# Kernel tuning notes

Measured on AMD Instinct MI355X. Metric: run time of the kernel, lower is better.

## Reference

```python
import jax, jax.numpy as jnp
import numpy as np

N = 3000          # num_nodes
B = 1             # batch
T_IN = 12
T_OUT = 12
F_IN = 2
F_OUT = 2
HEADS = 8
HID = 32          # hidden_dim (GAT out channels, LSTM hidden)
E = 32000         # directed edges (before self-loops)
NEG_SLOPE = 0.2   # PyG GATConv leaky_relu slope


def setup_inputs() -> dict:
    key = jax.random.key(0)
    ks = jax.random.split(key, 20)
    s = 0.1
    inp = {
        "X": jax.random.normal(ks[0], (B, N, T_IN, F_IN), jnp.float32),
        "edge_index": jax.random.randint(ks[1], (2, E), 0, N, dtype=jnp.int64),
        # GATConv params (shared lin for src/dst, concat=False -> bias of size HID)
        "gat_w": jax.random.normal(ks[2], (HEADS * HID, F_IN), jnp.float32) * s,
        "att_src": jax.random.normal(ks[3], (HEADS, HID), jnp.float32) * s,
        "att_dst": jax.random.normal(ks[4], (HEADS, HID), jnp.float32) * s,
        "gat_b": jax.random.normal(ks[5], (HID,), jnp.float32) * s,
        # 2-layer LSTM, PyTorch gate order (i, f, g, o)
        "w_ih0": jax.random.normal(ks[6], (4 * HID, HID), jnp.float32) * s,
        "w_hh0": jax.random.normal(ks[7], (4 * HID, HID), jnp.float32) * s,
        "b_ih0": jax.random.normal(ks[8], (4 * HID,), jnp.float32) * s,
        "b_hh0": jax.random.normal(ks[9], (4 * HID,), jnp.float32) * s,
        "w_ih1": jax.random.normal(ks[10], (4 * HID, HID), jnp.float32) * s,
        "w_hh1": jax.random.normal(ks[11], (4 * HID, HID), jnp.float32) * s,
        "b_ih1": jax.random.normal(ks[12], (4 * HID,), jnp.float32) * s,
        "b_hh1": jax.random.normal(ks[13], (4 * HID,), jnp.float32) * s,
        # final head: HID -> F_OUT * T_OUT
        "fc_w": jax.random.normal(ks[14], (F_OUT * T_OUT, HID), jnp.float32) * s,
        "fc_b": jax.random.normal(ks[15], (F_OUT * T_OUT,), jnp.float32) * s,
    }
    return inp


def _lstm_layer(xs, w_ih, w_hh, b_ih, b_hh):
    # xs: (T, BN, D) -> hidden states (T, BN, H)
    Hd = w_hh.shape[1]
    def step(carry, x):
        h, c = carry
        g = x @ w_ih.T + h @ w_hh.T + b_ih + b_hh
        i, f, gg, o = jnp.split(g, 4, axis=-1)
        c = jax.nn.sigmoid(f) * c + jax.nn.sigmoid(i) * jnp.tanh(gg)
        h = jax.nn.sigmoid(o) * jnp.tanh(c)
        return (h, c), h
    z = jnp.zeros((xs.shape[1], Hd), xs.dtype)
    _, hs = jax.lax.scan(step, (z, z), xs)
    return hs


def reference(X, edge_index, gat_w, att_src, att_dst, gat_b,
              w_ih0, w_hh0, b_ih0, b_hh0, w_ih1, w_hh1, b_ih1, b_hh1,
              fc_w, fc_b):
    Bb, Nn, T, F = X.shape
    BN = Bb * Nn
    H, C = att_src.shape

    # (T, BN, F), all timesteps processed at once (GAT params shared across t)
    Xr = X.transpose(2, 0, 1, 3).reshape(T, BN, F)
    h = (Xr @ gat_w.T).reshape(T, BN, H, C)          # shared lin for src/dst
    a_s = (h * att_src).sum(-1)                      # (T, BN, H)
    a_d = (h * att_dst).sum(-1)

    # add self-loops (PyG GATConv default) over all BN nodes
    loops = jnp.arange(BN, dtype=edge_index.dtype)
    src = jnp.concatenate([edge_index[0], loops])
    dst = jnp.concatenate([edge_index[1], loops])

    # edge attention logits, edge axis leading for segment ops: (Etot, T, H)
    e = jax.nn.leaky_relu(a_s[:, src] + a_d[:, dst], NEG_SLOPE)
    e = jnp.moveaxis(e, 1, 0)

    # segment softmax over incoming edges per destination node
    m = jax.ops.segment_max(e, dst, num_segments=BN)
    ex = jnp.exp(e - m[dst])
    den = jax.ops.segment_sum(ex, dst, num_segments=BN)
    alpha = ex / den[dst]                            # (Etot, T, H)

    h_node = jnp.moveaxis(h, 0, 1)                   # (BN, T, H, C)
    msg = alpha[..., None] * h_node[src]             # (Etot, T, H, C)
    agg = jax.ops.segment_sum(msg, dst, num_segments=BN)  # (BN, T, H, C)
    gat_out = agg.mean(2) + gat_b                    # concat=False -> head mean; (BN, T, C)

    # 2-layer LSTM over time
    xs = gat_out.transpose(1, 0, 2)                  # (T, BN, C)
    hs = _lstm_layer(xs, w_ih0, w_hh0, b_ih0, b_hh0)
    hs = _lstm_layer(hs, w_ih1, w_hh1, b_ih1, b_hh1)
    h_last = hs[-1]                                  # (BN, HID)

    out = h_last @ fc_w.T + fc_b                     # (BN, F_OUT*T_OUT)
    return out.reshape(Bb, Nn, T_OUT, F)
```

## Files before the change

### kernel.cpp

```cpp
#include <hip/hip_runtime.h>
#include <math.h>

#define N_NODES 3000
#define T_STEPS 12
#define F_INP 2
#define HEADS 8
#define HID 32
#define E_EDGES 32000
#define E_TOT (E_EDGES + N_NODES)
#define NEG_SLOPE 0.2f
#define OUT_F 24
#define CHUNKS 8
#define NT (N_NODES * T_STEPS)
#define WROW 33

__device__ __forceinline__ float sigm(float x) {
    return 1.0f / (1.0f + __expf(-x));
}
__device__ __forceinline__ float tanh_f(float x) {
    return 1.0f - 2.0f / (__expf(2.0f * x) + 1.0f);
}
__device__ __forceinline__ float rdlane(float v, int l) {
    return __int_as_float(__builtin_amdgcn_readlane(__float_as_int(v), l));
}

__global__ void k_init(int* __restrict__ deg,
                       const float* __restrict__ gat_w,
                       const float* __restrict__ att_src,
                       const float* __restrict__ att_dst,
                       float* __restrict__ proj,
                       const float* __restrict__ X,
                       float2* __restrict__ Xt) {
    int b = blockIdx.x;
    if (b < 12) {
        int i = b * 256 + threadIdx.x;
        if (i < N_NODES) deg[i] = 0;
    } else if (b == 12) {
        int tid = threadIdx.x;
        if (tid < 32) {
            int h = tid & 7, w = tid >> 3;
            const float* att = (w < 2) ? att_src : att_dst;
            int f = w & 1;
            float s = 0.0f;
            for (int c = 0; c < 32; c++)
                s += gat_w[((h * 32 + c) * 2) + f] * att[h * 32 + c];
            proj[w * 8 + h] = s;
        }
    } else {
        int i = (b - 13) * 256 + threadIdx.x;
        if (i < NT) {
            int n = i / T_STEPS, t = i - n * T_STEPS;
            float2 v = *(const float2*)&X[(size_t)i * 2];
            Xt[(size_t)t * N_NODES + n] = v;
        }
    }
}

__global__ void k_deg(const int* __restrict__ ei, int* __restrict__ deg) {
    int i = blockIdx.x * blockDim.x + threadIdx.x;
    if (i >= E_TOT) return;
    int d = (i < E_EDGES) ? ei[E_EDGES + i] : (i - E_EDGES);
    atomicAdd(&deg[d], 1);
}

__global__ __launch_bounds__(256) void k_scan(const int* __restrict__ deg,
                                              int* __restrict__ row_start,
                                              int* __restrict__ cursor) {
    __shared__ int part[256];
    int tid = threadIdx.x;
    const int CH = (N_NODES + 255) / 256;
    int base = tid * CH;
    int s = 0;
    for (int i = 0; i < CH; i++) {
        int idx = base + i;
        if (idx < N_NODES) s += deg[idx];
    }
    part[tid] = s;
    __syncthreads();
    if (tid == 0) {
        int run = 0;
        for (int i = 0; i < 256; i++) { int tmp = part[i]; part[i] = run; run += tmp; }
        row_start[N_NODES] = run;
    }
    __syncthreads();
    int off = part[tid];
    for (int i = 0; i < CH; i++) {
        int idx = base + i;
        if (idx < N_NODES) {
            row_start[idx] = off;
            cursor[idx] = off;
            off += deg[idx];
        }
    }
}

__global__ void k_scatter(const int* __restrict__ ei, int* __restrict__ cursor,
                          int* __restrict__ csr_src) {
    int i = blockIdx.x * blockDim.x + threadIdx.x;
    if (i >= E_TOT) return;
    int s, d;
    if (i < E_EDGES) { s = ei[i]; d = ei[E_EDGES + i]; }
    else             { s = i - E_EDGES; d = s; }
    int pos = atomicAdd(&cursor[d], 1);
    csr_src[pos] = s;
}

__global__ __launch_bounds__(256) void k_gat(const float2* __restrict__ Xt,
                                             const int* __restrict__ row_start,
                                             const int* __restrict__ csr_src,
                                             const float* __restrict__ proj,
                                             const float* __restrict__ gat_w,
                                             const float* __restrict__ gat_b,
                                             float* __restrict__ gat_out) {
    int pair = blockIdx.x * 4 + (threadIdx.x >> 6);
    int t = pair / N_NODES, n = pair - t * N_NODES;
    int lane = threadIdx.x & 63;
    int h = lane >> 3, slot = lane & 7;
    int rs = row_start[n];
    int deg = row_start[n + 1] - rs;
    const float2* Xp = Xt + (size_t)t * N_NODES;
    float ps0 = proj[h], ps1 = proj[8 + h];
    float pd0 = proj[16 + h], pd1 = proj[24 + h];
    float2 xd = Xp[n];
    float ad = fmaf(xd.x, pd0, xd.y * pd1);

    float x0c[CHUNKS], x1c[CHUNKS], sc[CHUNKS];
    float m = -1e30f;
    #pragma unroll
    for (int c = 0; c < CHUNKS; c++) {
        if (8 * c < deg) {
            int e = slot + 8 * c;
            int idx = rs + (e < deg ? e : deg - 1);
            int src = csr_src[idx];
            float2 xv = Xp[src];
            x0c[c] = xv.x; x1c[c] = xv.y;
            float s = fmaf(xv.x, ps0, fmaf(xv.y, ps1, ad));
            s = (s > 0.0f) ? s : NEG_SLOPE * s;
            sc[c] = (e < deg) ? s : -1e30f;
            m = fmaxf(m, sc[c]);
        } else { x0c[c] = 0.0f; x1c[c] = 0.0f; sc[c] = -1e30f; }
    }
    for (int e = 64 + slot; e < deg; e += 8) {
        float2 xv = Xp[csr_src[rs + e]];
        float s = fmaf(xv.x, ps0, fmaf(xv.y, ps1, ad));
        s = (s > 0.0f) ? s : NEG_SLOPE * s;
        m = fmaxf(m, s);
    }
    m = fmaxf(m, __shfl_xor(m, 1, 64));
    m = fmaxf(m, __shfl_xor(m, 2, 64));
    m = fmaxf(m, __shfl_xor(m, 4, 64));

    float den = 0.0f, S0 = 0.0f, S1 = 0.0f;
    #pragma unroll
    for (int c = 0; c < CHUNKS; c++) {
        if (8 * c < deg) {
            float a = __expf(sc[c] - m);
            den += a;
            S0 = fmaf(a, x0c[c], S0);
            S1 = fmaf(a, x1c[c], S1);
        }
    }
    for (int e = 64 + slot; e < deg; e += 8) {
        float2 xv = Xp[csr_src[rs + e]];
        float s = fmaf(xv.x, ps0, fmaf(xv.y, ps1, ad));
        s = (s > 0.0f) ? s : NEG_SLOPE * s;
        float a = __expf(s - m);
        den += a; S0 = fmaf(a, xv.x, S0); S1 = fmaf(a, xv.y, S1);
    }
    #pragma unroll
    for (int mm = 1; mm <= 4; mm <<= 1) {
        den += __shfl_xor(den, mm, 64);
        S0  += __shfl_xor(S0,  mm, 64);
        S1  += __shfl_xor(S1,  mm, 64);
    }
    float inv = 0.125f / den;
    float v0 = S0 * inv, v1 = S1 * inv;

    float a0[HEADS], a1[HEADS];
    #pragma unroll
    for (int hh = 0; hh < HEADS; hh++) {
        a0[hh] = rdlane(v0, hh * 8);
        a1[hh] = rdlane(v1, hh * 8);
    }

    int cc = lane & 31;
    float acc = gat_b[cc];
    #pragma unroll
    for (int hh = 0; hh < HEADS; hh++) {
        float2 g = *(const float2*)&gat_w[(hh * 32 + cc) * 2];
        acc = fmaf(a0[hh], g.x, fmaf(a1[hh], g.y, acc));
    }
    if (lane < 32)
        gat_out[((size_t)n * T_STEPS + t) * HID + cc] = acc;
}

__global__ __launch_bounds__(256, 3)
void k_lstm(const float* __restrict__ gat_out,
            const float* __restrict__ w_ih0,
            const float* __restrict__ w_hh0,
            const float* __restrict__ b_ih0,
            const float* __restrict__ b_hh0,
            const float* __restrict__ w_ih1,
            const float* __restrict__ w_hh1,
            const float* __restrict__ b_ih1,
            const float* __restrict__ b_hh1,
            const float* __restrict__ fc_w,
            const float* __restrict__ fc_b,
            float* __restrict__ out) {
    __shared__ float wl[128 * WROW];
    int tid = threadIdx.x;
    int lane = tid & 63;
    int n = blockIdx.x * 4 + (tid >> 6);
    int j = lane & 31, half = lane >> 5;
    int rowA = half * 64 + j;
    int rowB = rowA + 32;

    auto stage = [&](const float* __restrict__ src, int nfloats) {
        for (int base = tid * 4; base < nfloats; base += 1024) {
            float4 v = *(const float4*)&src[base];
            float* d = &wl[(base >> 5) * WROW + (base & 31)];
            d[0] = v.x; d[1] = v.y; d[2] = v.z; d[3] = v.w;
        }
    };
    auto loadrows = [&](float* wA, float* wB) {
        #pragma unroll
        for (int k = 0; k < 32; k++) wA[k] = wl[rowA * WROW + k];
        #pragma unroll
        for (int k = 0; k < 32; k++) wB[k] = wl[rowB * WROW + k];
    };

    float wA[32], wB[32];

    stage(w_ih0, 4096);
    __syncthreads();
    loadrows(wA, wB);
    float bA = b_ih0[rowA] + b_hh0[rowA];
    float bB = b_ih0[rowB] + b_hh0[rowB];
    float xrow[T_STEPS];
    #pragma unroll
    for (int t = 0; t < T_STEPS; t++)
        xrow[t] = gat_out[((size_t)n * T_STEPS + t) * HID + j];
    float gxa[T_STEPS], gxb[T_STEPS];
    #pragma unroll
    for (int t = 0; t < T_STEPS; t++) {
        float a = bA, b = bB;
        #pragma unroll
        for (int k = 0; k < 32; k++) {
            float xk = rdlane(xrow[t], k);
            a = fmaf(xk, wA[k], a);
            b = fmaf(xk, wB[k], b);
        }
        gxa[t] = a; gxb[t] = b;
    }
    __syncthreads();

    stage(w_hh0, 4096);
    __syncthreads();
    loadrows(wA, wB);
    float h = 0.0f, c = 0.0f;
    float h0s[T_STEPS];
    #pragma unroll
    for (int t = 0; t < T_STEPS; t++) {
        float gA0 = gxa[t], gB0 = gxb[t], gA1 = 0.0f, gB1 = 0.0f;
        #pragma unroll
        for (int k = 0; k < 16; k++) {
            float h0 = rdlane(h, k), h1 = rdlane(h, k + 16);
            gA0 = fmaf(h0, wA[k], gA0);      gA1 = fmaf(h1, wA[k + 16], gA1);
            gB0 = fmaf(h0, wB[k], gB0);      gB1 = fmaf(h1, wB[k + 16], gB1);
        }
        float gA = gA0 + gA1, gB = gB0 + gB1;
        float oA = __shfl_xor(gA, 32, 64);
        float oB = __shfl_xor(gB, 32, 64);
        float gi = half ? oA : gA;
        float gf = half ? oB : gB;
        float gg = half ? gA : oA;
        float go = half ? gB : oB;
        c = sigm(gf) * c + sigm(gi) * tanh_f(gg);
        h = sigm(go) * tanh_f(c);
        h0s[t] = h;
    }
    __syncthreads();

    stage(w_ih1, 4096);
    __syncthreads();
    loadrows(wA, wB);
    float bA1 = b_ih1[rowA] + b_hh1[rowA];
    float bB1 = b_ih1[rowB] + b_hh1[rowB];
    #pragma unroll
    for (int t = 0; t < T_STEPS; t++) {
        float a = bA1, b = bB1;
        #pragma unroll
        for (int k = 0; k < 32; k++) {
            float xk = rdlane(h0s[t], k);
            a = fmaf(xk, wA[k], a);
            b = fmaf(xk, wB[k], b);
        }
        gxa[t] = a; gxb[t] = b;
    }
    __syncthreads();

    stage(w_hh1, 4096);
    __syncthreads();
    loadrows(wA, wB);
    h = 0.0f; c = 0.0f;
    #pragma unroll
    for (int t = 0; t < T_STEPS; t++) {
        float gA0 = gxa[t], gB0 = gxb[t], gA1 = 0.0f, gB1 = 0.0f;
        #pragma unroll
        for (int k = 0; k < 16; k++) {
            float h0 = rdlane(h, k), h1 = rdlane(h, k + 16);
            gA0 = fmaf(h0, wA[k], gA0);      gA1 = fmaf(h1, wA[k + 16], gA1);
            gB0 = fmaf(h0, wB[k], gB0);      gB1 = fmaf(h1, wB[k + 16], gB1);
        }
        float gA = gA0 + gA1, gB = gB0 + gB1;
        float oA = __shfl_xor(gA, 32, 64);
        float oB = __shfl_xor(gB, 32, 64);
        float gi = half ? oA : gA;
        float gf = half ? oB : gB;
        float gg = half ? gA : oA;
        float go = half ? gB : oB;
        c = sigm(gf) * c + sigm(gi) * tanh_f(gg);
        h = sigm(go) * tanh_f(c);
    }
    __syncthreads();

    stage(fc_w, OUT_F * HID);
    __syncthreads();
    int o = (lane < OUT_F) ? lane : (OUT_F - 1);
    float acc = fc_b[o];
    #pragma unroll
    for (int k = 0; k < 32; k++) {
        float hk = rdlane(h, k);
        acc = fmaf(hk, wl[o * WROW + k], acc);
    }
    if (lane < OUT_F) out[(size_t)n * OUT_F + lane] = acc;
}

extern "C" void kernel_launch(void* const* d_in, const int* in_sizes, int n_in,
                              void* d_out, int out_size, void* d_ws, size_t ws_size,
                              hipStream_t stream) {
    (void)in_sizes; (void)n_in; (void)out_size; (void)ws_size;
    const float* X       = (const float*)d_in[0];
    const int*   ei      = (const int*)d_in[1];
    const float* gat_w   = (const float*)d_in[2];
    const float* att_src = (const float*)d_in[3];
    const float* att_dst = (const float*)d_in[4];
    const float* gat_b   = (const float*)d_in[5];
    const float* w_ih0   = (const float*)d_in[6];
    const float* w_hh0   = (const float*)d_in[7];
    const float* b_ih0   = (const float*)d_in[8];
    const float* b_hh0   = (const float*)d_in[9];
    const float* w_ih1   = (const float*)d_in[10];
    const float* w_hh1   = (const float*)d_in[11];
    const float* b_ih1   = (const float*)d_in[12];
    const float* b_hh1   = (const float*)d_in[13];
    const float* fc_w    = (const float*)d_in[14];
    const float* fc_b    = (const float*)d_in[15];
    float* out = (float*)d_out;

    char* ws = (char*)d_ws;
    size_t off = 0;
    auto alloc_f = [&](size_t n) { float* p = (float*)(ws + off); off += n * sizeof(float); return p; };
    auto alloc_i = [&](size_t n) { int* p = (int*)(ws + off); off += n * sizeof(int); return p; };

    float*  gat_out = alloc_f((size_t)NT * HID);
    float2* Xt      = (float2*)alloc_f((size_t)NT * 2);
    float*  proj    = alloc_f(32);
    int* deg       = alloc_i(N_NODES);
    int* row_start = alloc_i(N_NODES + 1);
    int* cursor    = alloc_i(N_NODES);
    int* csr_src   = alloc_i(E_TOT);

    k_init<<<13 + (NT + 255) / 256, 256, 0, stream>>>(deg, gat_w, att_src, att_dst,
                                                      proj, X, Xt);
    k_deg<<<(E_TOT + 255) / 256, 256, 0, stream>>>(ei, deg);
    k_scan<<<1, 256, 0, stream>>>(deg, row_start, cursor);
    k_scatter<<<(E_TOT + 255) / 256, 256, 0, stream>>>(ei, cursor, csr_src);
    k_gat<<<NT / 4, 256, 0, stream>>>(Xt, row_start, csr_src, proj,
                                      gat_w, gat_b, gat_out);
    k_lstm<<<N_NODES / 4, 256, 0, stream>>>(gat_out, w_ih0, w_hh0, b_ih0, b_hh0,
                                            w_ih1, w_hh1, b_ih1, b_hh1,
                                            fc_w, fc_b, out);
}
```

Measured before the change: 165.5 us.

## Fuse CSR build into single-block shared-memory kernel alongside transpose and projection

```diff
diff --git a/kernel.cpp b/kernel.cpp
--- a/kernel.cpp
+++ b/kernel.cpp
@@ -24,19 +24,67 @@
     return __int_as_float(__builtin_amdgcn_readlane(__float_as_int(v), l));
 }
 
-__global__ void k_init(int* __restrict__ deg,
-                       const float* __restrict__ gat_w,
-                       const float* __restrict__ att_src,
-                       const float* __restrict__ att_dst,
-                       float* __restrict__ proj,
-                       const float* __restrict__ X,
-                       float2* __restrict__ Xt) {
-    int b = blockIdx.x;
-    if (b < 12) {
-        int i = b * 256 + threadIdx.x;
-        if (i < N_NODES) deg[i] = 0;
-    } else if (b == 12) {
-        int tid = threadIdx.x;
+__global__ __launch_bounds__(1024) void k_graph(const int* __restrict__ ei,
+                                                const float* __restrict__ X,
+                                                const float* __restrict__ gat_w,
+                                                const float* __restrict__ att_src,
+                                                const float* __restrict__ att_dst,
+                                                float2* __restrict__ Xt,
+                                                float* __restrict__ proj,
+                                                int* __restrict__ row_start,
+                                                int* __restrict__ csr_src) {
+    int tid = threadIdx.x, b = blockIdx.x;
+    if (b == 0) {
+        __shared__ int sdeg[N_NODES];
+        __shared__ int wsum[17];
+        for (int i = tid; i < N_NODES; i += 1024) sdeg[i] = 0;
+        __syncthreads();
+        for (int i = tid; i < E_TOT; i += 1024) {
+            int d = (i < E_EDGES) ? ei[E_EDGES + i] : (i - E_EDGES);
+            atomicAdd(&sdeg[d], 1);
+        }
+        __syncthreads();
+        int base = tid * 3;
+        int d0 = (base     < N_NODES) ? sdeg[base]     : 0;
+        int d1 = (base + 1 < N_NODES) ? sdeg[base + 1] : 0;
+        int d2 = (base + 2 < N_NODES) ? sdeg[base + 2] : 0;
+        int s = d0 + d1 + d2;
+        int incl = s;
+        #pragma unroll
+        for (int dlt = 1; dlt < 64; dlt <<= 1) {
+            int v = __shfl_up(incl, dlt, 64);
+            if ((tid & 63) >= dlt) incl += v;
+        }
+        int wid = tid >> 6;
+        if ((tid & 63) == 63) wsum[wid] = incl;
+        __syncthreads();
+        if (tid == 0) {
+            int run = 0;
+            #pragma unroll
+            for (int w = 0; w < 16; w++) { int t2 = wsum[w]; wsum[w] = run; run += t2; }
+        }
+        __syncthreads();
+        int off = wsum[wid] + (incl - s);
+        if (base     < N_NODES) { row_start[base]     = off;           sdeg[base]     = off; }
+        if (base + 1 < N_NODES) { row_start[base + 1] = off + d0;      sdeg[base + 1] = off + d0; }
+        if (base + 2 < N_NODES) { row_start[base + 2] = off + d0 + d1; sdeg[base + 2] = off + d0 + d1; }
+        if (tid == 0) row_start[N_NODES] = E_TOT;
+        __syncthreads();
+        for (int i = tid; i < E_TOT; i += 1024) {
+            int s2, d;
+            if (i < E_EDGES) { s2 = ei[i]; d = ei[E_EDGES + i]; }
+            else             { s2 = i - E_EDGES; d = s2; }
+            int pos = atomicAdd(&sdeg[d], 1);
+            csr_src[pos] = s2;
+        }
+    } else if (b <= 36) {
+        int i = (b - 1) * 1024 + tid;
+        if (i < NT) {
+            int n = i / T_STEPS, t = i - n * T_STEPS;
+            float2 v = *(const float2*)&X[(size_t)i * 2];
+            Xt[(size_t)t * N_NODES + n] = v;
+        }
+    } else {
         if (tid < 32) {
             int h = tid & 7, w = tid >> 3;
             const float* att = (w < 2) ? att_src : att_dst;
@@ -46,63 +94,7 @@
                 s += gat_w[((h * 32 + c) * 2) + f] * att[h * 32 + c];
             proj[w * 8 + h] = s;
         }
-    } else {
-        int i = (b - 13) * 256 + threadIdx.x;
-        if (i < NT) {
-            int n = i / T_STEPS, t = i - n * T_STEPS;
-            float2 v = *(const float2*)&X[(size_t)i * 2];
-            Xt[(size_t)t * N_NODES + n] = v;
-        }
-    }
-}
-
-__global__ void k_deg(const int* __restrict__ ei, int* __restrict__ deg) {
-    int i = blockIdx.x * blockDim.x + threadIdx.x;
-    if (i >= E_TOT) return;
-    int d = (i < E_EDGES) ? ei[E_EDGES + i] : (i - E_EDGES);
-    atomicAdd(&deg[d], 1);
-}
-
-__global__ __launch_bounds__(256) void k_scan(const int* __restrict__ deg,
-                                              int* __restrict__ row_start,
-                                              int* __restrict__ cursor) {
-    __shared__ int part[256];
-    int tid = threadIdx.x;
-    const int CH = (N_NODES + 255) / 256;
-    int base = tid * CH;
-    int s = 0;
-    for (int i = 0; i < CH; i++) {
-        int idx = base + i;
-        if (idx < N_NODES) s += deg[idx];
-    }
-    part[tid] = s;
-    __syncthreads();
-    if (tid == 0) {
-        int run = 0;
-        for (int i = 0; i < 256; i++) { int tmp = part[i]; part[i] = run; run += tmp; }
-        row_start[N_NODES] = run;
-    }
-    __syncthreads();
-    int off = part[tid];
-    for (int i = 0; i < CH; i++) {
-        int idx = base + i;
-        if (idx < N_NODES) {
-            row_start[idx] = off;
-            cursor[idx] = off;
-            off += deg[idx];
-        }
-    }
-}
-
-__global__ void k_scatter(const int* __restrict__ ei, int* __restrict__ cursor,
-                          int* __restrict__ csr_src) {
-    int i = blockIdx.x * blockDim.x + threadIdx.x;
-    if (i >= E_TOT) return;
-    int s, d;
-    if (i < E_EDGES) { s = ei[i]; d = ei[E_EDGES + i]; }
-    else             { s = i - E_EDGES; d = s; }
-    int pos = atomicAdd(&cursor[d], 1);
-    csr_src[pos] = s;
+    }
 }
 
 __global__ __launch_bounds__(256) void k_gat(const float2* __restrict__ Xt,
@@ -194,7 +186,8 @@
         gat_out[((size_t)n * T_STEPS + t) * HID + cc] = acc;
 }
 
-__global__ __launch_bounds__(256, 3)
+__global__ __launch_bounds__(256)
+__attribute__((amdgpu_waves_per_eu(3, 3)))
 void k_lstm(const float* __restrict__ gat_out,
             const float* __restrict__ w_ih0,
             const float* __restrict__ w_hh0,
@@ -366,16 +359,11 @@
     float*  gat_out = alloc_f((size_t)NT * HID);
     float2* Xt      = (float2*)alloc_f((size_t)NT * 2);
     float*  proj    = alloc_f(32);
-    int* deg       = alloc_i(N_NODES);
     int* row_start = alloc_i(N_NODES + 1);
-    int* cursor    = alloc_i(N_NODES);
     int* csr_src   = alloc_i(E_TOT);
 
-    k_init<<<13 + (NT + 255) / 256, 256, 0, stream>>>(deg, gat_w, att_src, att_dst,
-                                                      proj, X, Xt);
-    k_deg<<<(E_TOT + 255) / 256, 256, 0, stream>>>(ei, deg);
-    k_scan<<<1, 256, 0, stream>>>(deg, row_start, cursor);
-    k_scatter<<<(E_TOT + 255) / 256, 256, 0, stream>>>(ei, cursor, csr_src);
+    k_graph<<<38, 1024, 0, stream>>>(ei, X, gat_w, att_src, att_dst,
+                                     Xt, proj, row_start, csr_src);
     k_gat<<<NT / 4, 256, 0, stream>>>(Xt, row_start, csr_src, proj,
                                       gat_w, gat_b, gat_out);
     k_lstm<<<N_NODES / 4, 256, 0, stream>>>(gat_out, w_ih0, w_hh0, b_ih0, b_hh0,
```

New measurement: 191.0 us. 15.4% more time.
